# Performance work log

Measured on AMD Instinct MI355X. Metric: run time of the kernel, lower is better.

## Reference

```python
import jax, jax.numpy as jnp
import numpy as np

C = 256          # in_channels == out_channels
K = 4            # number of parallel depthwise kernels
RED = 4          # SE reduction
KS = 3           # kernel size


def setup_inputs() -> dict:
    key = jax.random.key(0)
    ks = jax.random.split(key, 6)
    B, H, W = 32, 64, 64
    x = jax.random.normal(ks[0], (B, C, H, W), dtype=jnp.float32)
    # K depthwise kernels; per-conv torch weight shape = (C, 1, 3, 3)
    conv_w = jax.random.normal(ks[1], (K, C, 1, KS, KS), dtype=jnp.float32) * 0.1
    fc1_w = jax.random.normal(ks[2], (C // RED, C), dtype=jnp.float32) * (1.0 / np.sqrt(C))
    fc1_b = jnp.zeros((C // RED,), dtype=jnp.float32)
    fc2_w = jax.random.normal(ks[3], (K, C // RED), dtype=jnp.float32) * (1.0 / np.sqrt(C // RED))
    fc2_b = jnp.zeros((K,), dtype=jnp.float32)
    return {"x": x, "conv_w": conv_w, "fc1_w": fc1_w, "fc1_b": fc1_b,
            "fc2_w": fc2_w, "fc2_b": fc2_b}


def reference(x, conv_w, fc1_w, fc1_b, fc2_w, fc2_b):
    B, c, H, W = x.shape
    # --- attention branch: GAP -> fc -> relu -> fc -> softmax over K ---
    g = jnp.mean(x, axis=(2, 3))                       # [B, C]
    h = jax.nn.relu(g @ fc1_w.T + fc1_b)               # [B, C//r]
    attn = jax.nn.softmax(h @ fc2_w.T + fc2_b, axis=1) # [B, K]
    # --- all K depthwise convs as ONE grouped conv with K*C output channels ---
    # group i (input channel i) produces output channels [i*K:(i+1)*K],
    # so arrange weights as (C, K, 1, ks, ks) -> (C*K, 1, ks, ks)
    w_all = jnp.transpose(conv_w, (1, 0, 2, 3, 4)).reshape(c * K, 1, KS, KS)
    out = jax.lax.conv_general_dilated(
        x, w_all, window_strides=(1, 1), padding=[(1, 1), (1, 1)],
        feature_group_count=c,
        dimension_numbers=("NCHW", "OIHW", "NCHW"))    # [B, C*K, H, W]
    out = out.reshape(B, c, K, H, W)
    # attention-weighted sum over the K kernels
    return jnp.einsum("bckhw,bk->bchw", out, attn)
```

## Files before the change

kernel.cpp:

```cpp
#include <hip/hip_runtime.h>

#define CH 256
#define KK 4
#define HW 64
#define PLANE 4096
#define TS 67

typedef float fx4 __attribute__((ext_vector_type(4)));

__global__ __launch_bounds__(256) void gap_kernel(const float* __restrict__ x,
                                                  float* __restrict__ g) {
    int plane = blockIdx.x;
    const float4* p = (const float4*)(x + (size_t)plane * PLANE);
    float sum = 0.f;
    #pragma unroll
    for (int k = 0; k < 4; ++k) {
        float4 v = p[threadIdx.x + k * 256];
        sum += (v.x + v.y) + (v.z + v.w);
    }
    for (int off = 32; off > 0; off >>= 1)
        sum += __shfl_down(sum, off);
    __shared__ float ws[4];
    int lane = threadIdx.x & 63;
    int wid  = threadIdx.x >> 6;
    if (lane == 0) ws[wid] = sum;
    __syncthreads();
    if (threadIdx.x == 0)
        g[plane] = (ws[0] + ws[1] + ws[2] + ws[3]) * (1.f / PLANE);
}

__global__ __launch_bounds__(64) void attn_kernel(const float* __restrict__ g,
                            const float* __restrict__ fc1_w, const float* __restrict__ fc1_b,
                            const float* __restrict__ fc2_w, const float* __restrict__ fc2_b,
                            float* __restrict__ attn) {
    int b = blockIdx.x;
    int t = threadIdx.x;
    __shared__ float gs[CH];
    __shared__ float h[64];
    __shared__ float logit[KK];
    for (int i = t; i < CH; i += 64) gs[i] = g[b * CH + i];
    __syncthreads();
    {
        const float4* wr = (const float4*)(fc1_w + t * CH);
        const float4* gv = (const float4*)gs;
        float a0 = fc1_b[t], a1 = 0.f, a2 = 0.f, a3 = 0.f;
        #pragma unroll 4
        for (int i = 0; i < CH / 4; ++i) {
            float4 w4 = wr[i], g4 = gv[i];
            a0 = fmaf(w4.x, g4.x, a0);
            a1 = fmaf(w4.y, g4.y, a1);
            a2 = fmaf(w4.z, g4.z, a2);
            a3 = fmaf(w4.w, g4.w, a3);
        }
        h[t] = fmaxf((a0 + a1) + (a2 + a3), 0.f);
    }
    __syncthreads();
    if (t < KK) {
        const float4* w2 = (const float4*)(fc2_w + t * 64);
        const float4* hv = (const float4*)h;
        float a0 = fc2_b[t], a1 = 0.f, a2 = 0.f, a3 = 0.f;
        #pragma unroll
        for (int i = 0; i < 16; ++i) {
            float4 w4 = w2[i], h4 = hv[i];
            a0 = fmaf(w4.x, h4.x, a0);
            a1 = fmaf(w4.y, h4.y, a1);
            a2 = fmaf(w4.z, h4.z, a2);
            a3 = fmaf(w4.w, h4.w, a3);
        }
        logit[t] = (a0 + a1) + (a2 + a3);
    }
    __syncthreads();
    if (t == 0) {
        float m = fmaxf(fmaxf(logit[0], logit[1]), fmaxf(logit[2], logit[3]));
        float e[KK];
        float s = 0.f;
        #pragma unroll
        for (int k = 0; k < KK; ++k) { e[k] = __expf(logit[k] - m); s += e[k]; }
        float inv = 1.f / s;
        #pragma unroll
        for (int k = 0; k < KK; ++k) attn[b * KK + k] = e[k] * inv;
    }
}

__global__ __launch_bounds__(256) void dwconv_kernel(const float* __restrict__ x,
                              const float* __restrict__ conv_w,
                              const float* __restrict__ attn, float* __restrict__ out) {
    int plane = blockIdx.x;
    int b = plane >> 8;
    int c = plane & (CH - 1);
    __shared__ float tile[66 * TS];
    int t = threadIdx.x;

    float a0 = attn[b * KK + 0], a1 = attn[b * KK + 1],
          a2 = attn[b * KK + 2], a3 = attn[b * KK + 3];
    float w[9];
    #pragma unroll
    for (int j = 0; j < 9; ++j) {
        w[j] = a0 * conv_w[(0 * CH + c) * 9 + j]
             + a1 * conv_w[(1 * CH + c) * 9 + j]
             + a2 * conv_w[(2 * CH + c) * 9 + j]
             + a3 * conv_w[(3 * CH + c) * 9 + j];
    }

    for (int i = t; i < 260; i += 256) {
        int idx;
        if (i < 66)       idx = i;
        else if (i < 132) idx = 65 * TS + (i - 66);
        else if (i < 196) idx = (i - 131) * TS;
        else              idx = (i - 195) * TS + 65;
        tile[idx] = 0.f;
    }

    const float4* xp4 = (const float4*)(x + (size_t)plane * PLANE);
    #pragma unroll
    for (int k = 0; k < 4; ++k) {
        int idx = t + k * 256;
        int y   = idx >> 4;
        int xq  = (idx & 15) << 2;
        float4 v = xp4[idx];
        float* d = &tile[(y + 1) * TS + 1 + xq];
        d[0] = v.x; d[1] = v.y; d[2] = v.z; d[3] = v.w;
    }
    __syncthreads();

    int y0 = t >> 4;
    int xq = (t & 15) << 2;
    fx4* op4 = (fx4*)(out + (size_t)plane * PLANE);
    #pragma unroll
    for (int gi = 0; gi < 4; ++gi) {
        int y = y0 + gi * 16;
        float s0 = 0.f, s1 = 0.f, s2 = 0.f, s3 = 0.f;
        #pragma unroll
        for (int dy = 0; dy < 3; ++dy) {
            const float* r = &tile[(y + dy) * TS + xq];
            float e0 = r[0], e1 = r[1], e2 = r[2], e3 = r[3], e4 = r[4], e5 = r[5];
            float w0 = w[dy * 3], w1 = w[dy * 3 + 1], w2 = w[dy * 3 + 2];
            s0 = fmaf(e0, w0, fmaf(e1, w1, fmaf(e2, w2, s0)));
            s1 = fmaf(e1, w0, fmaf(e2, w1, fmaf(e3, w2, s1)));
            s2 = fmaf(e2, w0, fmaf(e3, w1, fmaf(e4, w2, s2)));
            s3 = fmaf(e3, w0, fmaf(e4, w1, fmaf(e5, w2, s3)));
        }
        fx4 res = {s0, s1, s2, s3};
        __builtin_nontemporal_store(res, &op4[(y << 4) + (t & 15)]);
    }
}

extern "C" void kernel_launch(void* const* d_in, const int* in_sizes, int n_in,
                              void* d_out, int out_size, void* d_ws, size_t ws_size,
                              hipStream_t stream) {
    const float* x      = (const float*)d_in[0];
    const float* conv_w = (const float*)d_in[1];
    const float* fc1_w  = (const float*)d_in[2];
    const float* fc1_b  = (const float*)d_in[3];
    const float* fc2_w  = (const float*)d_in[4];
    const float* fc2_b  = (const float*)d_in[5];
    float* out = (float*)d_out;

    int B = in_sizes[0] / (CH * HW * HW);

    float* g    = (float*)d_ws;
    float* attn = g + B * CH;

    gap_kernel <<<B * CH, 256, 0, stream>>>(x, g);
    attn_kernel<<<B, 64, 0, stream>>>(g, fc1_w, fc1_b, fc2_w, fc2_b, attn);
    dwconv_kernel<<<B * CH, 256, 0, stream>>>(x, conv_w, attn, out);
}
```

Before: 263.7 us.

## Fuse attention MLP into depthwise conv kernel, recomputing per block

Removes the separate attention kernel launch. Each conv block now recomputes the SE MLP and softmax for its batch from the pooled means, with the fc1 dot products split across all 256 threads. The x plane loads are issued up front so they overlap with that MLP work. The cost is redundant MLP computation in every one of the 8192 blocks, about 16K MACs plus fc1_w reads from cache each, extra syncs, and more LDS per block.

```diff
diff --git a/kernel.cpp b/kernel.cpp
--- a/kernel.cpp
+++ b/kernel.cpp
@@ -29,31 +29,55 @@
         g[plane] = (ws[0] + ws[1] + ws[2] + ws[3]) * (1.f / PLANE);
 }
 
-__global__ __launch_bounds__(64) void attn_kernel(const float* __restrict__ g,
-                            const float* __restrict__ fc1_w, const float* __restrict__ fc1_b,
-                            const float* __restrict__ fc2_w, const float* __restrict__ fc2_b,
-                            float* __restrict__ attn) {
-    int b = blockIdx.x;
-    int t = threadIdx.x;
+__global__ __launch_bounds__(256) void dwconv_kernel(const float* __restrict__ x,
+                              const float* __restrict__ g,
+                              const float* __restrict__ conv_w,
+                              const float* __restrict__ fc1_w, const float* __restrict__ fc1_b,
+                              const float* __restrict__ fc2_w, const float* __restrict__ fc2_b,
+                              float* __restrict__ out) {
+    int plane = blockIdx.x;
+    int b = plane >> 8;
+    int c = plane & (CH - 1);
+    __shared__ float tile[66 * TS];
     __shared__ float gs[CH];
+    __shared__ float red[256];
     __shared__ float h[64];
     __shared__ float logit[KK];
-    for (int i = t; i < CH; i += 64) gs[i] = g[b * CH + i];
+    int t = threadIdx.x;
+
+    const float4* xp4 = (const float4*)(x + (size_t)plane * PLANE);
+    float4 v0 = xp4[t], v1 = xp4[t + 256], v2 = xp4[t + 512], v3 = xp4[t + 768];
+
+    gs[t] = g[b * CH + t];
+
+    for (int i = t; i < 260; i += 256) {
+        int idx;
+        if (i < 66)       idx = i;
+        else if (i < 132) idx = 65 * TS + (i - 66);
+        else if (i < 196) idx = (i - 131) * TS;
+        else              idx = (i - 195) * TS + 65;
+        tile[idx] = 0.f;
+    }
     __syncthreads();
+
     {
-        const float4* wr = (const float4*)(fc1_w + t * CH);
-        const float4* gv = (const float4*)gs;
-        float a0 = fc1_b[t], a1 = 0.f, a2 = 0.f, a3 = 0.f;
-        #pragma unroll 4
-        for (int i = 0; i < CH / 4; ++i) {
+        int o = t & 63, pq = t >> 6;
+        const float4* wr = (const float4*)(fc1_w + o * CH + pq * 64);
+        const float4* gv = (const float4*)(gs + pq * 64);
+        float a0 = 0.f, a1 = 0.f, a2 = 0.f, a3 = 0.f;
+        #pragma unroll
+        for (int i = 0; i < 16; ++i) {
             float4 w4 = wr[i], g4 = gv[i];
             a0 = fmaf(w4.x, g4.x, a0);
             a1 = fmaf(w4.y, g4.y, a1);
             a2 = fmaf(w4.z, g4.z, a2);
             a3 = fmaf(w4.w, g4.w, a3);
         }
-        h[t] = fmaxf((a0 + a1) + (a2 + a3), 0.f);
+        red[t] = (a0 + a1) + (a2 + a3);
     }
+    __syncthreads();
+    if (t < 64)
+        h[t] = fmaxf(red[t] + red[64 + t] + red[128 + t] + red[192 + t] + fc1_b[t], 0.f);
     __syncthreads();
     if (t < KK) {
         const float4* w2 = (const float4*)(fc2_w + t * 64);
@@ -70,29 +94,23 @@
         logit[t] = (a0 + a1) + (a2 + a3);
     }
     __syncthreads();
-    if (t == 0) {
-        float m = fmaxf(fmaxf(logit[0], logit[1]), fmaxf(logit[2], logit[3]));
-        float e[KK];
-        float s = 0.f;
-        #pragma unroll
-        for (int k = 0; k < KK; ++k) { e[k] = __expf(logit[k] - m); s += e[k]; }
-        float inv = 1.f / s;
-        #pragma unroll
-        for (int k = 0; k < KK; ++k) attn[b * KK + k] = e[k] * inv;
+
+    float m  = fmaxf(fmaxf(logit[0], logit[1]), fmaxf(logit[2], logit[3]));
+    float e0 = __expf(logit[0] - m), e1 = __expf(logit[1] - m),
+          e2 = __expf(logit[2] - m), e3 = __expf(logit[3] - m);
+    float inv = 1.f / (e0 + e1 + e2 + e3);
+    float a0 = e0 * inv, a1 = e1 * inv, a2 = e2 * inv, a3 = e3 * inv;
+
+    #pragma unroll
+    for (int k = 0; k < 4; ++k) {
+        int idx = t + k * 256;
+        int y   = idx >> 4;
+        int xq  = (idx & 15) << 2;
+        float4 v = (k == 0) ? v0 : (k == 1) ? v1 : (k == 2) ? v2 : v3;
+        float* d = &tile[(y + 1) * TS + 1 + xq];
+        d[0] = v.x; d[1] = v.y; d[2] = v.z; d[3] = v.w;
     }
-}
 
-__global__ __launch_bounds__(256) void dwconv_kernel(const float* __restrict__ x,
-                              const float* __restrict__ conv_w,
-                              const float* __restrict__ attn, float* __restrict__ out) {
-    int plane = blockIdx.x;
-    int b = plane >> 8;
-    int c = plane & (CH - 1);
-    __shared__ float tile[66 * TS];
-    int t = threadIdx.x;
-
-    float a0 = attn[b * KK + 0], a1 = attn[b * KK + 1],
-          a2 = attn[b * KK + 2], a3 = attn[b * KK + 3];
     float w[9];
     #pragma unroll
     for (int j = 0; j < 9; ++j) {
@@ -100,26 +118,6 @@
              + a1 * conv_w[(1 * CH + c) * 9 + j]
              + a2 * conv_w[(2 * CH + c) * 9 + j]
              + a3 * conv_w[(3 * CH + c) * 9 + j];
-    }
-
-    for (int i = t; i < 260; i += 256) {
-        int idx;
-        if (i < 66)       idx = i;
-        else if (i < 132) idx = 65 * TS + (i - 66);
-        else if (i < 196) idx = (i - 131) * TS;
-        else              idx = (i - 195) * TS + 65;
-        tile[idx] = 0.f;
-    }
-
-    const float4* xp4 = (const float4*)(x + (size_t)plane * PLANE);
-    #pragma unroll
-    for (int k = 0; k < 4; ++k) {
-        int idx = t + k * 256;
-        int y   = idx >> 4;
-        int xq  = (idx & 15) << 2;
-        float4 v = xp4[idx];
-        float* d = &tile[(y + 1) * TS + 1 + xq];
-        d[0] = v.x; d[1] = v.y; d[2] = v.z; d[3] = v.w;
     }
     __syncthreads();
 
@@ -133,12 +131,12 @@
         #pragma unroll
         for (int dy = 0; dy < 3; ++dy) {
             const float* r = &tile[(y + dy) * TS + xq];
-            float e0 = r[0], e1 = r[1], e2 = r[2], e3 = r[3], e4 = r[4], e5 = r[5];
+            float e0_ = r[0], e1_ = r[1], e2_ = r[2], e3_ = r[3], e4_ = r[4], e5_ = r[5];
             float w0 = w[dy * 3], w1 = w[dy * 3 + 1], w2 = w[dy * 3 + 2];
-            s0 = fmaf(e0, w0, fmaf(e1, w1, fmaf(e2, w2, s0)));
-            s1 = fmaf(e1, w0, fmaf(e2, w1, fmaf(e3, w2, s1)));
-            s2 = fmaf(e2, w0, fmaf(e3, w1, fmaf(e4, w2, s2)));
-            s3 = fmaf(e3, w0, fmaf(e4, w1, fmaf(e5, w2, s3)));
+            s0 = fmaf(e0_, w0, fmaf(e1_, w1, fmaf(e2_, w2, s0)));
+            s1 = fmaf(e1_, w0, fmaf(e2_, w1, fmaf(e3_, w2, s1)));
+            s2 = fmaf(e2_, w0, fmaf(e3_, w1, fmaf(e4_, w2, s2)));
+            s3 = fmaf(e3_, w0, fmaf(e4_, w1, fmaf(e5_, w2, s3)));
         }
         fx4 res = {s0, s1, s2, s3};
         __builtin_nontemporal_store(res, &op4[(y << 4) + (t & 15)]);
@@ -158,10 +156,8 @@
 
     int B = in_sizes[0] / (CH * HW * HW);
 
-    float* g    = (float*)d_ws;
-    float* attn = g + B * CH;
+    float* g = (float*)d_ws;
 
-    gap_kernel <<<B * CH, 256, 0, stream>>>(x, g);
-    attn_kernel<<<B, 64, 0, stream>>>(g, fc1_w, fc1_b, fc2_w, fc2_b, attn);
-    dwconv_kernel<<<B * CH, 256, 0, stream>>>(x, conv_w, attn, out);
+    gap_kernel   <<<B * CH, 256, 0, stream>>>(x, g);
+    dwconv_kernel<<<B * CH, 256, 0, stream>>>(x, g, conv_w, fc1_w, fc1_b, fc2_w, fc2_b, out);
 }
```

New measurement: 296.4 us. +12.4%, slower.

## Use unpadded float4 LDS tile with shuffle halos and row-sliding register reuse

Applied to the files above, without the earlier changes.

The depthwise conv now stores the input plane as an unpadded float4 tile and drops the halo-zeroing loop. Each thread computes four consecutive output rows and keeps a sliding window of three input rows in registers, loading one new row per step. Left and right neighbours come from wave shuffles, and the global loads are issued before the weight mixing so their latency is hidden. This cuts LDS reads and scalar LDS writes, but adds shuffle instructions and boundary selects per row.

```diff
diff --git a/kernel.cpp b/kernel.cpp
--- a/kernel.cpp
+++ b/kernel.cpp
@@ -4,7 +4,6 @@
 #define KK 4
 #define HW 64
 #define PLANE 4096
-#define TS 67
 
 typedef float fx4 __attribute__((ext_vector_type(4)));
 
@@ -82,14 +81,19 @@
     }
 }
 
+struct R6 { float e0, e1, e2, e3, e4, e5; };
+
 __global__ __launch_bounds__(256) void dwconv_kernel(const float* __restrict__ x,
                               const float* __restrict__ conv_w,
                               const float* __restrict__ attn, float* __restrict__ out) {
     int plane = blockIdx.x;
     int b = plane >> 8;
     int c = plane & (CH - 1);
-    __shared__ float tile[66 * TS];
+    __shared__ float4 tile4[64 * 16];
     int t = threadIdx.x;
+
+    const float4* xp4 = (const float4*)(x + (size_t)plane * PLANE);
+    float4 v0 = xp4[t], v1 = xp4[t + 256], v2 = xp4[t + 512], v3 = xp4[t + 768];
 
     float a0 = attn[b * KK + 0], a1 = attn[b * KK + 1],
           a2 = attn[b * KK + 2], a3 = attn[b * KK + 3];
@@ -102,46 +106,48 @@
              + a3 * conv_w[(3 * CH + c) * 9 + j];
     }
 
-    for (int i = t; i < 260; i += 256) {
-        int idx;
-        if (i < 66)       idx = i;
-        else if (i < 132) idx = 65 * TS + (i - 66);
-        else if (i < 196) idx = (i - 131) * TS;
-        else              idx = (i - 195) * TS + 65;
-        tile[idx] = 0.f;
-    }
-
-    const float4* xp4 = (const float4*)(x + (size_t)plane * PLANE);
-    #pragma unroll
-    for (int k = 0; k < 4; ++k) {
-        int idx = t + k * 256;
-        int y   = idx >> 4;
-        int xq  = (idx & 15) << 2;
-        float4 v = xp4[idx];
-        float* d = &tile[(y + 1) * TS + 1 + xq];
-        d[0] = v.x; d[1] = v.y; d[2] = v.z; d[3] = v.w;
-    }
+    tile4[t] = v0; tile4[t + 256] = v1; tile4[t + 512] = v2; tile4[t + 768] = v3;
     __syncthreads();
 
-    int y0 = t >> 4;
-    int xq = (t & 15) << 2;
+    int c4 = t & 15;
+    int ys = t >> 4;
+    int r0 = ys << 2;
+
+    auto load_row = [&](int ry) -> R6 {
+        float4 f = {0.f, 0.f, 0.f, 0.f};
+        if ((unsigned)ry < 64u) f = tile4[(ry << 4) + c4];
+        float lw = __shfl_up(f.w, 1);
+        float rx = __shfl_down(f.x, 1);
+        R6 r;
+        r.e0 = (c4 == 0)  ? 0.f : lw;
+        r.e1 = f.x; r.e2 = f.y; r.e3 = f.z; r.e4 = f.w;
+        r.e5 = (c4 == 15) ? 0.f : rx;
+        return r;
+    };
+    auto acc_row = [&](const R6& r, float w0, float w1, float w2,
+                       float& s0, float& s1, float& s2, float& s3) {
+        s0 = fmaf(r.e0, w0, fmaf(r.e1, w1, fmaf(r.e2, w2, s0)));
+        s1 = fmaf(r.e1, w0, fmaf(r.e2, w1, fmaf(r.e3, w2, s1)));
+        s2 = fmaf(r.e2, w0, fmaf(r.e3, w1, fmaf(r.e4, w2, s2)));
+        s3 = fmaf(r.e3, w0, fmaf(r.e4, w1, fmaf(r.e5, w2, s3)));
+    };
+
+    R6 ra = load_row(r0 - 1);
+    R6 rb = load_row(r0);
+    R6 rc = load_row(r0 + 1);
+
     fx4* op4 = (fx4*)(out + (size_t)plane * PLANE);
     #pragma unroll
-    for (int gi = 0; gi < 4; ++gi) {
-        int y = y0 + gi * 16;
+    for (int j = 0; j < 4; ++j) {
         float s0 = 0.f, s1 = 0.f, s2 = 0.f, s3 = 0.f;
-        #pragma unroll
-        for (int dy = 0; dy < 3; ++dy) {
-            const float* r = &tile[(y + dy) * TS + xq];
-            float e0 = r[0], e1 = r[1], e2 = r[2], e3 = r[3], e4 = r[4], e5 = r[5];
-            float w0 = w[dy * 3], w1 = w[dy * 3 + 1], w2 = w[dy * 3 + 2];
-            s0 = fmaf(e0, w0, fmaf(e1, w1, fmaf(e2, w2, s0)));
-            s1 = fmaf(e1, w0, fmaf(e2, w1, fmaf(e3, w2, s1)));
-            s2 = fmaf(e2, w0, fmaf(e3, w1, fmaf(e4, w2, s2)));
-            s3 = fmaf(e3, w0, fmaf(e4, w1, fmaf(e5, w2, s3)));
+        acc_row(ra, w[0], w[1], w[2], s0, s1, s2, s3);
+        acc_row(rb, w[3], w[4], w[5], s0, s1, s2, s3);
+        acc_row(rc, w[6], w[7], w[8], s0, s1, s2, s3);
+        fx4 res = {s0, s1, s2, s3};
+        __builtin_nontemporal_store(res, &op4[((r0 + j) << 4) + c4]);
+        if (j < 3) {
+            ra = rb; rb = rc; rc = load_row(r0 + 2 + j);
         }
-        fx4 res = {s0, s1, s2, s3};
-        __builtin_nontemporal_store(res, &op4[(y << 4) + (t & 15)]);
     }
 }
 
```

Result: no change. 262.4 us (-0.5%).
